# Optimization experiments

Hardware: AMD Instinct MI355X
Metric: run time of the kernel (lower is better)

Reference implementation:

```python
import jax, jax.numpy as jnp
import numpy as np

N = 50000      # nodes
E = 600000     # edges
B = 64         # graphs in batch
DIN = 128      # input_dim
DH = 128       # hidden_dim
P = 32         # perm_length
C = 2          # num_classes
K = 2          # TAGConv hops (DGL default)


def setup_inputs() -> dict:
    key = jax.random.key(0)
    ks = jax.random.split(key, 12)
    h = jax.random.normal(ks[0], (N, DIN), dtype=jnp.float32)
    src = jax.random.randint(ks[1], (E,), 0, N, dtype=jnp.int64)
    dst = jax.random.randint(ks[2], (E,), 0, N, dtype=jnp.int64)
    graph_ids = jnp.sort(jax.random.randint(ks[3], (N,), 0, B, dtype=jnp.int64))
    perm_features = jax.random.normal(ks[4], (B, P), dtype=jnp.float32)
    s1 = 1.0 / np.sqrt((K + 1) * DIN)
    s2 = 1.0 / np.sqrt((K + 1) * DH)
    sc = 1.0 / np.sqrt(DH + P)
    W1 = jax.random.uniform(ks[5], ((K + 1) * DIN, DH), jnp.float32, -s1, s1)
    b1 = jax.random.uniform(ks[6], (DH,), jnp.float32, -s1, s1)
    W2 = jax.random.uniform(ks[7], ((K + 1) * DH, DH), jnp.float32, -s2, s2)
    b2 = jax.random.uniform(ks[8], (DH,), jnp.float32, -s2, s2)
    Wc = jax.random.uniform(ks[9], (DH + P, C), jnp.float32, -sc, sc)
    bc = jax.random.uniform(ks[10], (C,), jnp.float32, -sc, sc)
    return {"h": h, "src": src, "dst": dst, "graph_ids": graph_ids,
            "perm_features": perm_features, "W1": W1, "b1": b1,
            "W2": W2, "b2": b2, "Wc": Wc, "bc": bc}


def _tag_conv(x, src, dst, norm, W, b):
    feats = [x]
    for _ in range(K):
        m = jax.ops.segment_sum((feats[-1] * norm)[src], dst, num_segments=N)
        feats.append(m * norm)
    return jnp.concatenate(feats, axis=-1) @ W + b


def reference(h, src, dst, graph_ids, perm_features, W1, b1, W2, b2, Wc, bc):
    # symmetric norm from in-degrees, clamped at 1 (DGL convention)
    deg = jax.ops.segment_sum(jnp.ones((E,), h.dtype), dst, num_segments=N)
    norm = jnp.where(deg < 1.0, 1.0, deg)[:, None] ** -0.5  # [N,1]
    x = jax.nn.relu(_tag_conv(h, src, dst, norm, W1, b1))
    x = _tag_conv(x, src, dst, norm, W2, b2)
    # mean_nodes over batched graph
    sums = jax.ops.segment_sum(x, graph_ids, num_segments=B)          # [B,DH]
    cnt = jax.ops.segment_sum(jnp.ones((N,), x.dtype), graph_ids, num_segments=B)
    hg = sums / jnp.maximum(cnt, 1.0)[:, None]
    combined = jnp.concatenate([hg, perm_features], axis=1)           # [B,DH+P]
    return combined @ Wc + bc
```

## Files before the change

### kernel.cpp

```cpp
#include <hip/hip_runtime.h>

#define N_NODES 50000
#define N_EDGES 600000
#define B_GRAPHS 64
#define DH 128
#define PFEAT 32
#define NCLS 2
#define SCAN_BLOCKS ((N_NODES + 255) / 256)
#define NPAD (N_NODES + 128)
#define NCVT4 (N_NODES * 128 / 4)
#define WELEMS (384 * 128)

typedef __attribute__((ext_vector_type(8))) short short8v;
typedef __attribute__((ext_vector_type(4))) float float4v;
typedef __attribute__((ext_vector_type(4))) unsigned int uint4v;

__device__ __forceinline__ unsigned int f2bf(float f) {
    unsigned int u = __float_as_uint(f);
    return (u + 0x7FFFu + ((u >> 16) & 1u)) >> 16;
}
__device__ __forceinline__ float bflo(unsigned int p) { return __uint_as_float(p << 16); }
__device__ __forceinline__ float bfhi(unsigned int p) { return __uint_as_float(p & 0xFFFF0000u); }

__global__ void k_init(const float* __restrict__ h, unsigned short* __restrict__ h_bf,
                       const float* __restrict__ W1, const float* __restrict__ W2,
                       unsigned short* __restrict__ Wt1, unsigned short* __restrict__ Wt2,
                       int* __restrict__ deg, float* __restrict__ gsum,
                       int* __restrict__ gstart) {
    int t = blockIdx.x * 256 + threadIdx.x;
    if (t < NCVT4) {
        float4 v = ((const float4*)h)[t];
        unsigned int lo = f2bf(v.x) | (f2bf(v.y) << 16);
        unsigned int hi = f2bf(v.z) | (f2bf(v.w) << 16);
        uint2 r; r.x = lo; r.y = hi;
        ((uint2*)h_bf)[t] = r;
    }
    if (t < 2 * WELEMS) {
        bool second = (t >= WELEMS);
        int idx = second ? t - WELEMS : t;
        const float* W = second ? W2 : W1;
        unsigned short* Wt = second ? Wt2 : Wt1;
        int k = idx >> 7, c = idx & 127;
        Wt[c * 384 + k] = (unsigned short)f2bf(W[idx]);
    }
    if (t < N_NODES) deg[t] = 0;
    if (t < B_GRAPHS * DH) gsum[t] = 0.f;
    if (t < B_GRAPHS) gstart[t] = -1;
}

__global__ void k_deg_bound(const int* __restrict__ dst, const int* __restrict__ gid,
                            int* __restrict__ deg, int* __restrict__ epos,
                            int* __restrict__ gstart) {
    int t = blockIdx.x * 256 + threadIdx.x;
    if (t < N_EDGES) {
        int pos = atomicAdd(&deg[dst[t]], 1);
        epos[t] = pos;
    }
    int n = t - N_EDGES;
    if (n >= 0 && n < N_NODES) {
        int g = gid[n];
        if (n == 0 || gid[n - 1] != g) gstart[g] = n;
    }
}

__global__ void k_norm_bsum(const int* __restrict__ deg, float* __restrict__ norm,
                            int* __restrict__ bsum) {
    __shared__ int s[256];
    int i = blockIdx.x * 256 + threadIdx.x;
    int d = (i < N_NODES) ? deg[i] : 0;
    if (i < N_NODES) norm[i] = rsqrtf((float)(d < 1 ? 1 : d));
    s[threadIdx.x] = d;
    __syncthreads();
    for (int off = 128; off > 0; off >>= 1) {
        if (threadIdx.x < off) s[threadIdx.x] += s[threadIdx.x + off];
        __syncthreads();
    }
    if (threadIdx.x == 0) bsum[blockIdx.x] = s[0];
}

__global__ void k_scan2(const int* __restrict__ deg, const int* __restrict__ bsum,
                        int* __restrict__ row_ptr) {
    __shared__ int sb[256];
    __shared__ int s[256];
    int bv = (threadIdx.x < SCAN_BLOCKS) ? bsum[threadIdx.x] : 0;
    sb[threadIdx.x] = bv;
    int i = blockIdx.x * 256 + threadIdx.x;
    int v = (i < N_NODES) ? deg[i] : 0;
    s[threadIdx.x] = v;
    __syncthreads();
    for (int off = 1; off < 256; off <<= 1) {
        int tb = (threadIdx.x >= off) ? sb[threadIdx.x - off] : 0;
        int t = (threadIdx.x >= off) ? s[threadIdx.x - off] : 0;
        __syncthreads();
        sb[threadIdx.x] += tb;
        s[threadIdx.x] += t;
        __syncthreads();
    }
    int block_off = (blockIdx.x == 0) ? 0 : sb[blockIdx.x - 1];
    if (i < N_NODES) row_ptr[i + 1] = s[threadIdx.x] + block_off;
    if (i == 0) row_ptr[0] = 0;
}

__global__ void k_scatter(const int* __restrict__ src, const int* __restrict__ dst,
                          const int* __restrict__ row_ptr, const int* __restrict__ epos,
                          int* __restrict__ col) {
    int e = blockIdx.x * blockDim.x + threadIdx.x;
    if (e < N_EDGES) {
        int d = dst[e];
        col[row_ptr[d] + epos[e]] = src[e];
    }
}

__global__ __launch_bounds__(256) void k_spmm(const unsigned short* __restrict__ fin,
                                              const float* __restrict__ norm,
                                              const int* __restrict__ row_ptr,
                                              const int* __restrict__ col,
                                              unsigned short* __restrict__ fout) {
    int wave = threadIdx.x >> 6;
    int lane = threadIdx.x & 63;
    int grp = lane >> 4;
    int l15 = lane & 15;
    int v = blockIdx.x * 4 + wave;
    if (v >= N_NODES) return;
    int beg = row_ptr[v], end = row_ptr[v + 1];

    float a0[8], a1[8], a2[8], a3[8];
#pragma unroll
    for (int j = 0; j < 8; ++j) { a0[j] = 0.f; a1[j] = 0.f; a2[j] = 0.f; a3[j] = 0.f; }

    for (int base = beg; base < end; base += 16) {
        int e0 = base + grp;
        int e1 = e0 + 4, e2 = e0 + 8, e3 = e0 + 12;
        int last = end - 1;
        int c0 = (e0 < end) ? e0 : last;
        int c1 = (e1 < end) ? e1 : last;
        int c2 = (e2 < end) ? e2 : last;
        int c3 = (e3 < end) ? e3 : last;
        int u0 = col[c0], u1 = col[c1], u2 = col[c2], u3 = col[c3];
        uint4v r0 = *(const uint4v*)(fin + (size_t)u0 * 128 + l15 * 8);
        uint4v r1 = *(const uint4v*)(fin + (size_t)u1 * 128 + l15 * 8);
        uint4v r2 = *(const uint4v*)(fin + (size_t)u2 * 128 + l15 * 8);
        uint4v r3 = *(const uint4v*)(fin + (size_t)u3 * 128 + l15 * 8);
        float w0 = (e0 < end) ? norm[u0] : 0.f;
        float w1 = (e1 < end) ? norm[u1] : 0.f;
        float w2 = (e2 < end) ? norm[u2] : 0.f;
        float w3 = (e3 < end) ? norm[u3] : 0.f;
#pragma unroll
        for (int q = 0; q < 4; ++q) {
            a0[2 * q]     = fmaf(bflo(r0[q]), w0, a0[2 * q]);
            a0[2 * q + 1] = fmaf(bfhi(r0[q]), w0, a0[2 * q + 1]);
            a1[2 * q]     = fmaf(bflo(r1[q]), w1, a1[2 * q]);
            a1[2 * q + 1] = fmaf(bfhi(r1[q]), w1, a1[2 * q + 1]);
            a2[2 * q]     = fmaf(bflo(r2[q]), w2, a2[2 * q]);
            a2[2 * q + 1] = fmaf(bfhi(r2[q]), w2, a2[2 * q + 1]);
            a3[2 * q]     = fmaf(bflo(r3[q]), w3, a3[2 * q]);
            a3[2 * q + 1] = fmaf(bfhi(r3[q]), w3, a3[2 * q + 1]);
        }
    }

#pragma unroll
    for (int j = 0; j < 8; ++j) {
        float s = (a0[j] + a1[j]) + (a2[j] + a3[j]);
        s += __shfl_xor(s, 16, 64);
        s += __shfl_xor(s, 32, 64);
        a0[j] = s;
    }
    if (grp == 0) {
        float nv = norm[v];
        uint4v o;
#pragma unroll
        for (int q = 0; q < 4; ++q)
            o[q] = f2bf(a0[2 * q] * nv) | (f2bf(a0[2 * q + 1] * nv) << 16);
        *(uint4v*)(fout + (size_t)v * 128 + l15 * 8) = o;
    }
}

template <bool RELU, bool POOL>
__global__ __launch_bounds__(256) void k_gemm_mfma(const unsigned short* __restrict__ A0,
                                                   const unsigned short* __restrict__ A1,
                                                   const unsigned short* __restrict__ A2,
                                                   const unsigned short* __restrict__ Wt,
                                                   const float* __restrict__ bias,
                                                   unsigned short* __restrict__ out,
                                                   const int* __restrict__ gid,
                                                   float* __restrict__ gsum) {
    __shared__ float red4[4][128];
    int tid = threadIdx.x;
    int lane = tid & 63;
    int wid = tid >> 6;
    int l15 = lane & 15;
    int lk = lane >> 4;
    int n0 = blockIdx.x * 128;
    int rbase = n0 + wid * 32;

    float4v acc[2][8];
#pragma unroll
    for (int rt = 0; rt < 2; ++rt)
#pragma unroll
        for (int ct = 0; ct < 8; ++ct)
#pragma unroll
            for (int i = 0; i < 4; ++i) acc[rt][ct][i] = 0.f;

    const unsigned short* Aseg[3] = {A0, A1, A2};
#pragma unroll
    for (int ks = 0; ks < 12; ++ks) {
        const unsigned short* A = Aseg[ks >> 2];
        int kloc = (ks & 3) * 32 + lk * 8;
        short8v a0 = *(const short8v*)(A + (size_t)(rbase + l15) * 128 + kloc);
        short8v a1 = *(const short8v*)(A + (size_t)(rbase + 16 + l15) * 128 + kloc);
        const unsigned short* wp = Wt + (size_t)l15 * 384 + ks * 32 + lk * 8;
#pragma unroll
        for (int ct = 0; ct < 8; ++ct) {
            short8v b = *(const short8v*)(wp + (size_t)ct * 16 * 384);
            acc[0][ct] = __builtin_amdgcn_mfma_f32_16x16x32_bf16(a0, b, acc[0][ct], 0, 0, 0);
            acc[1][ct] = __builtin_amdgcn_mfma_f32_16x16x32_bf16(a1, b, acc[1][ct], 0, 0, 0);
        }
    }

    if (!POOL) {
        float bj[8];
#pragma unroll
        for (int ct = 0; ct < 8; ++ct) bj[ct] = bias[ct * 16 + l15];
#pragma unroll
        for (int rt = 0; rt < 2; ++rt)
#pragma unroll
            for (int i = 0; i < 4; ++i) {
                int row = rbase + rt * 16 + lk * 4 + i;
                if (row < N_NODES) {
#pragma unroll
                    for (int ct = 0; ct < 8; ++ct) {
                        float v = acc[rt][ct][i] + bj[ct];
                        if (RELU) v = fmaxf(v, 0.f);
                        out[(size_t)row * 128 + ct * 16 + l15] = (unsigned short)f2bf(v);
                    }
                }
            }
    } else {
        int gr[2][4];
#pragma unroll
        for (int rt = 0; rt < 2; ++rt)
#pragma unroll
            for (int i = 0; i < 4; ++i) {
                int row = rbase + rt * 16 + lk * 4 + i;
                gr[rt][i] = (row < N_NODES) ? gid[row] : -1;
            }
        int lastrow = n0 + 127;
        if (lastrow >= N_NODES) lastrow = N_NODES - 1;
        int gfirst = gid[n0];
        int glast = gid[lastrow];
        for (int g = gfirst; g <= glast; ++g) {
            float p[8];
#pragma unroll
            for (int ct = 0; ct < 8; ++ct) {
                float s = 0.f;
#pragma unroll
                for (int rt = 0; rt < 2; ++rt)
#pragma unroll
                    for (int i = 0; i < 4; ++i)
                        if (gr[rt][i] == g) s += acc[rt][ct][i];
                p[ct] = s;
            }
#pragma unroll
            for (int ct = 0; ct < 8; ++ct) {
                p[ct] += __shfl_xor(p[ct], 16, 64);
                p[ct] += __shfl_xor(p[ct], 32, 64);
            }
            if (lane < 16) {
#pragma unroll
                for (int ct = 0; ct < 8; ++ct) red4[wid][ct * 16 + lane] = p[ct];
            }
            __syncthreads();
            if (tid < 128) {
                float s = red4[0][tid] + red4[1][tid] + red4[2][tid] + red4[3][tid];
                atomicAdd(&gsum[g * 128 + tid], s);
            }
            __syncthreads();
        }
    }
}

__global__ void k_final(const float* __restrict__ gsum, const int* __restrict__ gstart,
                        const float* __restrict__ b2, const float* __restrict__ perm,
                        const float* __restrict__ Wc, const float* __restrict__ bc,
                        float* __restrict__ out) {
    int t = threadIdx.x;
    if (t >= B_GRAPHS * NCLS) return;
    int b = t / NCLS, c = t % NCLS;
    int s = gstart[b];
    float cf = 1.f;
    bool nonempty = (s >= 0);
    if (nonempty) {
        int nxt = N_NODES;
        for (int j = b + 1; j < B_GRAPHS; ++j) {
            int sj = gstart[j];
            if (sj >= 0) { nxt = sj; break; }
        }
        int cnt = nxt - s;
        cf = (cnt < 1) ? 1.f : (float)cnt;
    }
    float acc = bc[c];
    for (int d = 0; d < DH; ++d) {
        float hg = gsum[b * 128 + d] / cf + (nonempty ? b2[d] : 0.f);
        acc += hg * Wc[d * NCLS + c];
    }
    for (int p = 0; p < PFEAT; ++p) acc += perm[b * PFEAT + p] * Wc[(DH + p) * NCLS + c];
    out[t] = acc;
}

extern "C" void kernel_launch(void* const* d_in, const int* in_sizes, int n_in,
                              void* d_out, int out_size, void* d_ws, size_t ws_size,
                              hipStream_t stream) {
    const float* h    = (const float*)d_in[0];
    const int*   src  = (const int*)d_in[1];
    const int*   dst  = (const int*)d_in[2];
    const int*   gid  = (const int*)d_in[3];
    const float* perm = (const float*)d_in[4];
    const float* W1   = (const float*)d_in[5];
    const float* b1   = (const float*)d_in[6];
    const float* W2   = (const float*)d_in[7];
    const float* b2   = (const float*)d_in[8];
    const float* Wc   = (const float*)d_in[9];
    const float* bc   = (const float*)d_in[10];
    float* out = (float*)d_out;

    char* ws = (char*)d_ws;
    size_t off = 0;
    auto alloc = [&](size_t bytes) {
        void* p = ws + off;
        off = (off + bytes + 255) & ~(size_t)255;
        return p;
    };
    int*   deg     = (int*)alloc(N_NODES * 4);
    int*   row_ptr = (int*)alloc((N_NODES + 1) * 4);
    int*   col     = (int*)alloc(N_EDGES * 4);
    int*   epos    = (int*)alloc(N_EDGES * 4);
    int*   bsum    = (int*)alloc(SCAN_BLOCKS * 4);
    float* norm    = (float*)alloc(N_NODES * 4);
    unsigned short* h_bf = (unsigned short*)alloc((size_t)NPAD * 128 * 2);
    unsigned short* f1   = (unsigned short*)alloc((size_t)NPAD * 128 * 2);
    unsigned short* f2   = (unsigned short*)alloc((size_t)NPAD * 128 * 2);
    unsigned short* x2   = (unsigned short*)alloc((size_t)NPAD * 128 * 2);
    unsigned short* Wt1  = (unsigned short*)alloc(384 * 128 * 2);
    unsigned short* Wt2  = (unsigned short*)alloc(384 * 128 * 2);
    float* gsum    = (float*)alloc(B_GRAPHS * 128 * 4);
    int*   gstart  = (int*)alloc(B_GRAPHS * 4);

    k_init<<<(NCVT4 + 255) / 256, 256, 0, stream>>>(h, h_bf, W1, W2, Wt1, Wt2,
                                                    deg, gsum, gstart);
    k_deg_bound<<<(N_EDGES + N_NODES + 255) / 256, 256, 0, stream>>>(dst, gid, deg, epos, gstart);
    k_norm_bsum<<<SCAN_BLOCKS, 256, 0, stream>>>(deg, norm, bsum);
    k_scan2<<<SCAN_BLOCKS, 256, 0, stream>>>(deg, bsum, row_ptr);
    k_scatter<<<(N_EDGES + 255) / 256, 256, 0, stream>>>(src, dst, row_ptr, epos, col);

    int spmm_grid = (N_NODES + 3) / 4;
    int gemm_grid = (N_NODES + 127) / 128;

    k_spmm<<<spmm_grid, 256, 0, stream>>>(h_bf, norm, row_ptr, col, f1);
    k_spmm<<<spmm_grid, 256, 0, stream>>>(f1, norm, row_ptr, col, f2);
    k_gemm_mfma<true, false><<<gemm_grid, 256, 0, stream>>>(h_bf, f1, f2, Wt1, b1, x2, gid, gsum);

    k_spmm<<<spmm_grid, 256, 0, stream>>>(x2, norm, row_ptr, col, f1);
    k_spmm<<<spmm_grid, 256, 0, stream>>>(f1, norm, row_ptr, col, f2);
    k_gemm_mfma<false, true><<<gemm_grid, 256, 0, stream>>>(x2, f1, f2, Wt2, nullptr, nullptr, gid, gsum);

    k_final<<<1, 128, 0, stream>>>(gsum, gstart, b2, perm, Wc, bc, out);
}
```

Baseline: 248.2 us.

## Halve GEMM row tile and fold final classifier into last-block of pooled GEMM

The MFMA GEMM now gives each block 64 rows instead of 128, one 16-row tile per wave, which doubles the grid and cuts accumulator registers. The separate single-block classifier kernel is removed. The pooled GEMM now uses an atomic completion counter with a threadfence, and the last block to finish computes the mean-pool and the linear head. This saves one kernel launch and gives more parallelism, at the cost of more weight reloads per row and more atomic pooling traffic.

```diff
diff --git a/kernel.cpp b/kernel.cpp
--- a/kernel.cpp
+++ b/kernel.cpp
@@ -10,6 +10,7 @@
 #define NPAD (N_NODES + 128)
 #define NCVT4 (N_NODES * 128 / 4)
 #define WELEMS (384 * 128)
+#define GEMM_GRID ((N_NODES + 63) / 64)
 
 typedef __attribute__((ext_vector_type(8))) short short8v;
 typedef __attribute__((ext_vector_type(4))) float float4v;
@@ -26,7 +27,7 @@
                        const float* __restrict__ W1, const float* __restrict__ W2,
                        unsigned short* __restrict__ Wt1, unsigned short* __restrict__ Wt2,
                        int* __restrict__ deg, float* __restrict__ gsum,
-                       int* __restrict__ gstart) {
+                       int* __restrict__ gstart, int* __restrict__ done) {
     int t = blockIdx.x * 256 + threadIdx.x;
     if (t < NCVT4) {
         float4 v = ((const float4*)h)[t];
@@ -46,6 +47,7 @@
     if (t < N_NODES) deg[t] = 0;
     if (t < B_GRAPHS * DH) gsum[t] = 0.f;
     if (t < B_GRAPHS) gstart[t] = -1;
+    if (t == 0) *done = 0;
 }
 
 __global__ void k_deg_bound(const int* __restrict__ dst, const int* __restrict__ gid,
@@ -183,37 +185,41 @@
                                                    const float* __restrict__ bias,
                                                    unsigned short* __restrict__ out,
                                                    const int* __restrict__ gid,
-                                                   float* __restrict__ gsum) {
+                                                   float* __restrict__ gsum,
+                                                   int* __restrict__ done,
+                                                   const int* __restrict__ gstart,
+                                                   const float* __restrict__ b2,
+                                                   const float* __restrict__ perm,
+                                                   const float* __restrict__ Wc,
+                                                   const float* __restrict__ bc,
+                                                   float* __restrict__ fout) {
     __shared__ float red4[4][128];
+    __shared__ int lastFlag;
     int tid = threadIdx.x;
     int lane = tid & 63;
     int wid = tid >> 6;
     int l15 = lane & 15;
     int lk = lane >> 4;
-    int n0 = blockIdx.x * 128;
-    int rbase = n0 + wid * 32;
-
-    float4v acc[2][8];
-#pragma unroll
-    for (int rt = 0; rt < 2; ++rt)
-#pragma unroll
-        for (int ct = 0; ct < 8; ++ct)
-#pragma unroll
-            for (int i = 0; i < 4; ++i) acc[rt][ct][i] = 0.f;
+    int n0 = blockIdx.x * 64;
+    int rbase = n0 + wid * 16;
+
+    float4v acc[8];
+#pragma unroll
+    for (int ct = 0; ct < 8; ++ct)
+#pragma unroll
+        for (int i = 0; i < 4; ++i) acc[ct][i] = 0.f;
 
     const unsigned short* Aseg[3] = {A0, A1, A2};
 #pragma unroll
     for (int ks = 0; ks < 12; ++ks) {
         const unsigned short* A = Aseg[ks >> 2];
         int kloc = (ks & 3) * 32 + lk * 8;
-        short8v a0 = *(const short8v*)(A + (size_t)(rbase + l15) * 128 + kloc);
-        short8v a1 = *(const short8v*)(A + (size_t)(rbase + 16 + l15) * 128 + kloc);
+        short8v a = *(const short8v*)(A + (size_t)(rbase + l15) * 128 + kloc);
         const unsigned short* wp = Wt + (size_t)l15 * 384 + ks * 32 + lk * 8;
 #pragma unroll
         for (int ct = 0; ct < 8; ++ct) {
             short8v b = *(const short8v*)(wp + (size_t)ct * 16 * 384);
-            acc[0][ct] = __builtin_amdgcn_mfma_f32_16x16x32_bf16(a0, b, acc[0][ct], 0, 0, 0);
-            acc[1][ct] = __builtin_amdgcn_mfma_f32_16x16x32_bf16(a1, b, acc[1][ct], 0, 0, 0);
+            acc[ct] = __builtin_amdgcn_mfma_f32_16x16x32_bf16(a, b, acc[ct], 0, 0, 0);
         }
     }
 
@@ -222,31 +228,27 @@
 #pragma unroll
         for (int ct = 0; ct < 8; ++ct) bj[ct] = bias[ct * 16 + l15];
 #pragma unroll
-        for (int rt = 0; rt < 2; ++rt)
-#pragma unroll
-            for (int i = 0; i < 4; ++i) {
-                int row = rbase + rt * 16 + lk * 4 + i;
-                if (row < N_NODES) {
-#pragma unroll
-                    for (int ct = 0; ct < 8; ++ct) {
-                        float v = acc[rt][ct][i] + bj[ct];
-                        if (RELU) v = fmaxf(v, 0.f);
-                        out[(size_t)row * 128 + ct * 16 + l15] = (unsigned short)f2bf(v);
-                    }
+        for (int i = 0; i < 4; ++i) {
+            int row = rbase + lk * 4 + i;
+            if (row < N_NODES) {
+#pragma unroll
+                for (int ct = 0; ct < 8; ++ct) {
+                    float v = acc[ct][i] + bj[ct];
+                    if (RELU) v = fmaxf(v, 0.f);
+                    out[(size_t)row * 128 + ct * 16 + l15] = (unsigned short)f2bf(v);
                 }
             }
+        }
     } else {
-        int gr[2][4];
-#pragma unroll
-        for (int rt = 0; rt < 2; ++rt)
-#pragma unroll
-            for (int i = 0; i < 4; ++i) {
-                int row = rbase + rt * 16 + lk * 4 + i;
-                gr[rt][i] = (row < N_NODES) ? gid[row] : -1;
-            }
-        int lastrow = n0 + 127;
+        int gr[4];
+#pragma unroll
+        for (int i = 0; i < 4; ++i) {
+            int row = rbase + lk * 4 + i;
+            gr[i] = (row < N_NODES) ? gid[row] : -1;
+        }
+        int lastrow = n0 + 63;
         if (lastrow >= N_NODES) lastrow = N_NODES - 1;
-        int gfirst = gid[n0];
+        int gfirst = gid[n0 < N_NODES ? n0 : N_NODES - 1];
         int glast = gid[lastrow];
         for (int g = gfirst; g <= glast; ++g) {
             float p[8];
@@ -254,10 +256,8 @@
             for (int ct = 0; ct < 8; ++ct) {
                 float s = 0.f;
 #pragma unroll
-                for (int rt = 0; rt < 2; ++rt)
-#pragma unroll
-                    for (int i = 0; i < 4; ++i)
-                        if (gr[rt][i] == g) s += acc[rt][ct][i];
+                for (int i = 0; i < 4; ++i)
+                    if (gr[i] == g) s += acc[ct][i];
                 p[ct] = s;
             }
 #pragma unroll
@@ -276,35 +276,40 @@
             }
             __syncthreads();
         }
-    }
-}
-
-__global__ void k_final(const float* __restrict__ gsum, const int* __restrict__ gstart,
-                        const float* __restrict__ b2, const float* __restrict__ perm,
-                        const float* __restrict__ Wc, const float* __restrict__ bc,
-                        float* __restrict__ out) {
-    int t = threadIdx.x;
-    if (t >= B_GRAPHS * NCLS) return;
-    int b = t / NCLS, c = t % NCLS;
-    int s = gstart[b];
-    float cf = 1.f;
-    bool nonempty = (s >= 0);
-    if (nonempty) {
-        int nxt = N_NODES;
-        for (int j = b + 1; j < B_GRAPHS; ++j) {
-            int sj = gstart[j];
-            if (sj >= 0) { nxt = sj; break; }
-        }
-        int cnt = nxt - s;
-        cf = (cnt < 1) ? 1.f : (float)cnt;
-    }
-    float acc = bc[c];
-    for (int d = 0; d < DH; ++d) {
-        float hg = gsum[b * 128 + d] / cf + (nonempty ? b2[d] : 0.f);
-        acc += hg * Wc[d * NCLS + c];
-    }
-    for (int p = 0; p < PFEAT; ++p) acc += perm[b * PFEAT + p] * Wc[(DH + p) * NCLS + c];
-    out[t] = acc;
+
+        __threadfence();
+        if (tid == 0) {
+            int old = atomicAdd(done, 1);
+            lastFlag = (old == (int)gridDim.x - 1) ? 1 : 0;
+        }
+        __syncthreads();
+        if (lastFlag) {
+            __threadfence();
+            if (tid < B_GRAPHS * NCLS) {
+                int b = tid >> 1, c = tid & 1;
+                int s = gstart[b];
+                float cf = 1.f;
+                bool nonempty = (s >= 0);
+                if (nonempty) {
+                    int nxt = N_NODES;
+                    for (int j = b + 1; j < B_GRAPHS; ++j) {
+                        int sj = gstart[j];
+                        if (sj >= 0) { nxt = sj; break; }
+                    }
+                    int cnt = nxt - s;
+                    cf = (cnt < 1) ? 1.f : (float)cnt;
+                }
+                float acc2 = bc[c];
+                for (int d = 0; d < DH; ++d) {
+                    float hg = gsum[b * 128 + d] / cf + (nonempty ? b2[d] : 0.f);
+                    acc2 += hg * Wc[d * NCLS + c];
+                }
+                for (int p = 0; p < PFEAT; ++p)
+                    acc2 += perm[b * PFEAT + p] * Wc[(DH + p) * NCLS + c];
+                fout[tid] = acc2;
+            }
+        }
+    }
 }
 
 extern "C" void kernel_launch(void* const* d_in, const int* in_sizes, int n_in,
@@ -344,24 +349,26 @@
     unsigned short* Wt2  = (unsigned short*)alloc(384 * 128 * 2);
     float* gsum    = (float*)alloc(B_GRAPHS * 128 * 4);
     int*   gstart  = (int*)alloc(B_GRAPHS * 4);
+    int*   done    = (int*)alloc(4);
 
     k_init<<<(NCVT4 + 255) / 256, 256, 0, stream>>>(h, h_bf, W1, W2, Wt1, Wt2,
-                                                    deg, gsum, gstart);
+                                                    deg, gsum, gstart, done);
     k_deg_bound<<<(N_EDGES + N_NODES + 255) / 256, 256, 0, stream>>>(dst, gid, deg, epos, gstart);
     k_norm_bsum<<<SCAN_BLOCKS, 256, 0, stream>>>(deg, norm, bsum);
     k_scan2<<<SCAN_BLOCKS, 256, 0, stream>>>(deg, bsum, row_ptr);
     k_scatter<<<(N_EDGES + 255) / 256, 256, 0, stream>>>(src, dst, row_ptr, epos, col);
 
     int spmm_grid = (N_NODES + 3) / 4;
-    int gemm_grid = (N_NODES + 127) / 128;
 
     k_spmm<<<spmm_grid, 256, 0, stream>>>(h_bf, norm, row_ptr, col, f1);
     k_spmm<<<spmm_grid, 256, 0, stream>>>(f1, norm, row_ptr, col, f2);
-    k_gemm_mfma<true, false><<<gemm_grid, 256, 0, stream>>>(h_bf, f1, f2, Wt1, b1, x2, gid, gsum);
+    k_gemm_mfma<true, false><<<GEMM_GRID, 256, 0, stream>>>(
+        h_bf, f1, f2, Wt1, b1, x2, gid, gsum, done,
+        nullptr, nullptr, nullptr, nullptr, nullptr, nullptr);
 
     k_spmm<<<spmm_grid, 256, 0, stream>>>(x2, norm, row_ptr, col, f1);
     k_spmm<<<spmm_grid, 256, 0, stream>>>(f1, norm, row_ptr, col, f2);
-    k_gemm_mfma<false, true><<<gemm_grid, 256, 0, stream>>>(x2, f1, f2, Wt2, nullptr, nullptr, gid, gsum);
-
-    k_final<<<1, 128, 0, stream>>>(gsum, gstart, b2, perm, Wc, bc, out);
-}
+    k_gemm_mfma<false, true><<<GEMM_GRID, 256, 0, stream>>>(
+        x2, f1, f2, Wt2, nullptr, nullptr, gid, gsum, done,
+        gstart, b2, perm, Wc, bc, out);
+}
```

New measurement: 332.5 us. 1.34x slower.

## Store features pre-scaled by norm to drop per-edge norm gathers in SpMM

Applied to the files above, without the earlier changes.

Rewrites the propagation in a rescaled basis. Every feature buffer now holds values multiplied by norm[v], so the SpMM inner loop becomes a plain sum with no per-edge norm[u] gather and no FMA weight. The output is scaled by norm^2, and the GEMM epilogues compensate: the bias is multiplied by norm, and the pooling step multiplies by rnorm = sqrt(deg). Invalid edge slots are redirected to a zeroed padding row. The h conversion is fused into the scatter kernel. This adds an rnorm array and extra bf16 rounding of pre-scaled values, which may change accuracy slightly.

```diff
diff --git a/kernel.cpp b/kernel.cpp
--- a/kernel.cpp
+++ b/kernel.cpp
@@ -22,19 +22,13 @@
 __device__ __forceinline__ float bflo(unsigned int p) { return __uint_as_float(p << 16); }
 __device__ __forceinline__ float bfhi(unsigned int p) { return __uint_as_float(p & 0xFFFF0000u); }
 
-__global__ void k_init(const float* __restrict__ h, unsigned short* __restrict__ h_bf,
-                       const float* __restrict__ W1, const float* __restrict__ W2,
+__global__ void k_init(const float* __restrict__ W1, const float* __restrict__ W2,
                        unsigned short* __restrict__ Wt1, unsigned short* __restrict__ Wt2,
                        int* __restrict__ deg, float* __restrict__ gsum,
-                       int* __restrict__ gstart) {
+                       int* __restrict__ gstart,
+                       unsigned short* __restrict__ h_bf, unsigned short* __restrict__ f1,
+                       unsigned short* __restrict__ f2, unsigned short* __restrict__ x2) {
     int t = blockIdx.x * 256 + threadIdx.x;
-    if (t < NCVT4) {
-        float4 v = ((const float4*)h)[t];
-        unsigned int lo = f2bf(v.x) | (f2bf(v.y) << 16);
-        unsigned int hi = f2bf(v.z) | (f2bf(v.w) << 16);
-        uint2 r; r.x = lo; r.y = hi;
-        ((uint2*)h_bf)[t] = r;
-    }
     if (t < 2 * WELEMS) {
         bool second = (t >= WELEMS);
         int idx = second ? t - WELEMS : t;
@@ -46,6 +40,11 @@
     if (t < N_NODES) deg[t] = 0;
     if (t < B_GRAPHS * DH) gsum[t] = 0.f;
     if (t < B_GRAPHS) gstart[t] = -1;
+    if (t < 4 * 32) {
+        unsigned short* bufs[4] = {h_bf, f1, f2, x2};
+        uint2 z; z.x = 0u; z.y = 0u;
+        ((uint2*)(bufs[t >> 5] + (size_t)N_NODES * 128))[t & 31] = z;
+    }
 }
 
 __global__ void k_deg_bound(const int* __restrict__ dst, const int* __restrict__ gid,
@@ -64,11 +63,15 @@
 }
 
 __global__ void k_norm_bsum(const int* __restrict__ deg, float* __restrict__ norm,
-                            int* __restrict__ bsum) {
+                            float* __restrict__ rnorm, int* __restrict__ bsum) {
     __shared__ int s[256];
     int i = blockIdx.x * 256 + threadIdx.x;
     int d = (i < N_NODES) ? deg[i] : 0;
-    if (i < N_NODES) norm[i] = rsqrtf((float)(d < 1 ? 1 : d));
+    if (i < N_NODES) {
+        int dc = d < 1 ? 1 : d;
+        norm[i] = rsqrtf((float)dc);
+        rnorm[i] = sqrtf((float)dc);
+    }
     s[threadIdx.x] = d;
     __syncthreads();
     for (int off = 128; off > 0; off >>= 1) {
@@ -101,13 +104,23 @@
     if (i == 0) row_ptr[0] = 0;
 }
 
-__global__ void k_scatter(const int* __restrict__ src, const int* __restrict__ dst,
-                          const int* __restrict__ row_ptr, const int* __restrict__ epos,
-                          int* __restrict__ col) {
-    int e = blockIdx.x * blockDim.x + threadIdx.x;
-    if (e < N_EDGES) {
-        int d = dst[e];
-        col[row_ptr[d] + epos[e]] = src[e];
+__global__ void k_scatter_cvt(const int* __restrict__ src, const int* __restrict__ dst,
+                              const int* __restrict__ row_ptr, const int* __restrict__ epos,
+                              int* __restrict__ col, const float* __restrict__ h,
+                              const float* __restrict__ norm,
+                              unsigned short* __restrict__ h_bf) {
+    int t = blockIdx.x * 256 + threadIdx.x;
+    if (t < N_EDGES) {
+        int d = dst[t];
+        col[row_ptr[d] + epos[t]] = src[t];
+    }
+    if (t < NCVT4) {
+        float4 v = ((const float4*)h)[t];
+        float nv = norm[t >> 5];
+        unsigned int lo = f2bf(v.x * nv) | (f2bf(v.y * nv) << 16);
+        unsigned int hi = f2bf(v.z * nv) | (f2bf(v.w * nv) << 16);
+        uint2 r; r.x = lo; r.y = hi;
+        ((uint2*)h_bf)[t] = r;
     }
 }
 
@@ -137,24 +150,24 @@
         int c2 = (e2 < end) ? e2 : last;
         int c3 = (e3 < end) ? e3 : last;
         int u0 = col[c0], u1 = col[c1], u2 = col[c2], u3 = col[c3];
+        u0 = (e0 < end) ? u0 : N_NODES;
+        u1 = (e1 < end) ? u1 : N_NODES;
+        u2 = (e2 < end) ? u2 : N_NODES;
+        u3 = (e3 < end) ? u3 : N_NODES;
         uint4v r0 = *(const uint4v*)(fin + (size_t)u0 * 128 + l15 * 8);
         uint4v r1 = *(const uint4v*)(fin + (size_t)u1 * 128 + l15 * 8);
         uint4v r2 = *(const uint4v*)(fin + (size_t)u2 * 128 + l15 * 8);
         uint4v r3 = *(const uint4v*)(fin + (size_t)u3 * 128 + l15 * 8);
-        float w0 = (e0 < end) ? norm[u0] : 0.f;
-        float w1 = (e1 < end) ? norm[u1] : 0.f;
-        float w2 = (e2 < end) ? norm[u2] : 0.f;
-        float w3 = (e3 < end) ? norm[u3] : 0.f;
 #pragma unroll
         for (int q = 0; q < 4; ++q) {
-            a0[2 * q]     = fmaf(bflo(r0[q]), w0, a0[2 * q]);
-            a0[2 * q + 1] = fmaf(bfhi(r0[q]), w0, a0[2 * q + 1]);
-            a1[2 * q]     = fmaf(bflo(r1[q]), w1, a1[2 * q]);
-            a1[2 * q + 1] = fmaf(bfhi(r1[q]), w1, a1[2 * q + 1]);
-            a2[2 * q]     = fmaf(bflo(r2[q]), w2, a2[2 * q]);
-            a2[2 * q + 1] = fmaf(bfhi(r2[q]), w2, a2[2 * q + 1]);
-            a3[2 * q]     = fmaf(bflo(r3[q]), w3, a3[2 * q]);
-            a3[2 * q + 1] = fmaf(bfhi(r3[q]), w3, a3[2 * q + 1]);
+            a0[2 * q]     += bflo(r0[q]);
+            a0[2 * q + 1] += bfhi(r0[q]);
+            a1[2 * q]     += bflo(r1[q]);
+            a1[2 * q + 1] += bfhi(r1[q]);
+            a2[2 * q]     += bflo(r2[q]);
+            a2[2 * q + 1] += bfhi(r2[q]);
+            a3[2 * q]     += bflo(r3[q]);
+            a3[2 * q + 1] += bfhi(r3[q]);
         }
     }
 
@@ -167,10 +180,11 @@
     }
     if (grp == 0) {
         float nv = norm[v];
+        float s2 = nv * nv;
         uint4v o;
 #pragma unroll
         for (int q = 0; q < 4; ++q)
-            o[q] = f2bf(a0[2 * q] * nv) | (f2bf(a0[2 * q + 1] * nv) << 16);
+            o[q] = f2bf(a0[2 * q] * s2) | (f2bf(a0[2 * q + 1] * s2) << 16);
         *(uint4v*)(fout + (size_t)v * 128 + l15 * 8) = o;
     }
 }
@@ -183,7 +197,9 @@
                                                    const float* __restrict__ bias,
                                                    unsigned short* __restrict__ out,
                                                    const int* __restrict__ gid,
-                                                   float* __restrict__ gsum) {
+                                                   float* __restrict__ gsum,
+                                                   const float* __restrict__ normv,
+                                                   const float* __restrict__ rnorm) {
     __shared__ float red4[4][128];
     int tid = threadIdx.x;
     int lane = tid & 63;
@@ -227,9 +243,10 @@
             for (int i = 0; i < 4; ++i) {
                 int row = rbase + rt * 16 + lk * 4 + i;
                 if (row < N_NODES) {
+                    float nv = normv[row];
 #pragma unroll
                     for (int ct = 0; ct < 8; ++ct) {
-                        float v = acc[rt][ct][i] + bj[ct];
+                        float v = acc[rt][ct][i] + nv * bj[ct];
                         if (RELU) v = fmaxf(v, 0.f);
                         out[(size_t)row * 128 + ct * 16 + l15] = (unsigned short)f2bf(v);
                     }
@@ -237,12 +254,15 @@
             }
     } else {
         int gr[2][4];
+        float rn[2][4];
 #pragma unroll
         for (int rt = 0; rt < 2; ++rt)
 #pragma unroll
             for (int i = 0; i < 4; ++i) {
                 int row = rbase + rt * 16 + lk * 4 + i;
-                gr[rt][i] = (row < N_NODES) ? gid[row] : -1;
+                bool ok = (row < N_NODES);
+                gr[rt][i] = ok ? gid[row] : -1;
+                rn[rt][i] = ok ? rnorm[row] : 0.f;
             }
         int lastrow = n0 + 127;
         if (lastrow >= N_NODES) lastrow = N_NODES - 1;
@@ -257,7 +277,7 @@
                 for (int rt = 0; rt < 2; ++rt)
 #pragma unroll
                     for (int i = 0; i < 4; ++i)
-                        if (gr[rt][i] == g) s += acc[rt][ct][i];
+                        if (gr[rt][i] == g) s += rn[rt][i] * acc[rt][ct][i];
                 p[ct] = s;
             }
 #pragma unroll
@@ -336,6 +356,7 @@
     int*   epos    = (int*)alloc(N_EDGES * 4);
     int*   bsum    = (int*)alloc(SCAN_BLOCKS * 4);
     float* norm    = (float*)alloc(N_NODES * 4);
+    float* rnorm   = (float*)alloc(N_NODES * 4);
     unsigned short* h_bf = (unsigned short*)alloc((size_t)NPAD * 128 * 2);
     unsigned short* f1   = (unsigned short*)alloc((size_t)NPAD * 128 * 2);
     unsigned short* f2   = (unsigned short*)alloc((size_t)NPAD * 128 * 2);
@@ -345,23 +366,27 @@
     float* gsum    = (float*)alloc(B_GRAPHS * 128 * 4);
     int*   gstart  = (int*)alloc(B_GRAPHS * 4);
 
-    k_init<<<(NCVT4 + 255) / 256, 256, 0, stream>>>(h, h_bf, W1, W2, Wt1, Wt2,
-                                                    deg, gsum, gstart);
+    k_init<<<(2 * WELEMS + 255) / 256, 256, 0, stream>>>(W1, W2, Wt1, Wt2,
+                                                         deg, gsum, gstart,
+                                                         h_bf, f1, f2, x2);
     k_deg_bound<<<(N_EDGES + N_NODES + 255) / 256, 256, 0, stream>>>(dst, gid, deg, epos, gstart);
-    k_norm_bsum<<<SCAN_BLOCKS, 256, 0, stream>>>(deg, norm, bsum);
+    k_norm_bsum<<<SCAN_BLOCKS, 256, 0, stream>>>(deg, norm, rnorm, bsum);
     k_scan2<<<SCAN_BLOCKS, 256, 0, stream>>>(deg, bsum, row_ptr);
-    k_scatter<<<(N_EDGES + 255) / 256, 256, 0, stream>>>(src, dst, row_ptr, epos, col);
+    k_scatter_cvt<<<(NCVT4 + 255) / 256, 256, 0, stream>>>(src, dst, row_ptr, epos, col,
+                                                           h, norm, h_bf);
 
     int spmm_grid = (N_NODES + 3) / 4;
     int gemm_grid = (N_NODES + 127) / 128;
 
     k_spmm<<<spmm_grid, 256, 0, stream>>>(h_bf, norm, row_ptr, col, f1);
     k_spmm<<<spmm_grid, 256, 0, stream>>>(f1, norm, row_ptr, col, f2);
-    k_gemm_mfma<true, false><<<gemm_grid, 256, 0, stream>>>(h_bf, f1, f2, Wt1, b1, x2, gid, gsum);
+    k_gemm_mfma<true, false><<<gemm_grid, 256, 0, stream>>>(h_bf, f1, f2, Wt1, b1, x2,
+                                                            gid, gsum, norm, rnorm);
 
     k_spmm<<<spmm_grid, 256, 0, stream>>>(x2, norm, row_ptr, col, f1);
     k_spmm<<<spmm_grid, 256, 0, stream>>>(f1, norm, row_ptr, col, f2);
-    k_gemm_mfma<false, true><<<gemm_grid, 256, 0, stream>>>(x2, f1, f2, Wt2, nullptr, nullptr, gid, gsum);
+    k_gemm_mfma<false, true><<<gemm_grid, 256, 0, stream>>>(x2, f1, f2, Wt2, nullptr, nullptr,
+                                                            gid, gsum, norm, rnorm);
 
     k_final<<<1, 128, 0, stream>>>(gsum, gstart, b2, perm, Wc, bc, out);
 }
```

Measured after the change: 244.1 us. About the same (-1.7%).
